# Kernel optimization log

Measured on AMD Instinct MI355X. Metric: run time of the kernel, lower is better.

Reference implementation:

```python
import jax, jax.numpy as jnp
import numpy as np

# eval_para constants (init_kwargs)
RM = 100.0          # r_max
RN = 1000           # r_dsc (radial grid points)
L_MAX = 2
PARA1 = 1.0
RD = RM / RN        # radial step
MR = int(RN * 0.1)  # matching radius index = 100
E_BATCH = 4096

R = jnp.linspace(RM / RN, RM, RN, dtype=jnp.float32).reshape(RN, 1, 1)      # r grid
L = jnp.arange(L_MAX + 1, dtype=jnp.float32).reshape(1, 1, -1)               # l values
FACT = jnp.asarray([np.prod([2 * li + 1 for li in range(lm + 1)])
                    for lm in range(L_MAX + 1)], dtype=jnp.float32)          # (2l+1)!! = [1,3,15]


def disc_solve(sol_init, factor):
    """4th-order Numerov-style recurrence, faithful to the torch loop
    (including the original operator precedence: the 1/(1 - 3/40 rd^2 f[i+4])
    divisor applies only to the sol[i] term)."""
    rd2 = RD * RD
    a = 2.0 + (13.0 / 15.0) * rd2 * factor
    b = -2.0 + (7.0 / 60.0) * rd2 * factor
    c = -1.0 + (3.0 / 40.0) * rd2 * factor
    d = 1.0 - (3.0 / 40.0) * rd2 * factor
    xs = (a[3:RN - 1], b[2:RN - 2], a[1:RN - 3], c[:RN - 4], d[4:])  # each [RN-4, E, L]

    def step(carry, x):
        s0, s1, s2, s3 = carry
        a3, b2, a1, c0, d4 = x
        new = s3 * a3 + s2 * b2 + s1 * a1 + s0 * c0 / d4
        return (s1, s2, s3, new), new

    init = (sol_init[0], sol_init[1], sol_init[2], sol_init[3])
    _, ys = jax.lax.scan(step, init, xs)
    return jnp.concatenate([sol_init[:4], ys], axis=0)


def derivative(f, at):
    # 4th-order backward finite difference
    return (25.0 * f[at] - 48.0 * f[at - 1] + 36.0 * f[at - 2]
            - 16.0 * f[at - 3] + 3.0 * f[at - 4]) / (12.0 * RD)


def integrate_sq(f, n):
    """Faithful port of EvalEig.integrate: n panels of width 4*RD starting at
    index 0 (the original ignores the start offset and leaves f[4i+2] unsquared)."""
    f0 = f[0:4 * n:4]
    f1 = f[1:4 * n + 1:4]
    f2 = f[2:4 * n + 2:4]
    f3 = f[3:4 * n + 3:4]
    f4 = f[4:4 * n + 4:4]
    return ((7.0 * (f0 ** 2 + f4 ** 2) + 32.0 * (f1 ** 2 + f3 ** 2)
             + 12.0 * f2) * (2.0 * RD / 45.0)).sum(0)


def _forward(init_energy):
    E = init_energy.shape[0]
    energy = jnp.broadcast_to(init_energy[:, None], (E, L_MAX + 1))  # [E, L]

    # diffeq_factor with coulomb potential -1/r
    e = energy[None]                                    # [1, E, L]
    factor = L * (L + 1.0) / R ** 2 + PARA1 * (-e - 1.0 / R)  # [RN, E, L]

    # u_zero series initial condition near r=0
    u0_init = jnp.broadcast_to(
        R ** (L + 1.0) + R ** (L + 2.0) / (2.0 * (L + 1.0)) * (-PARA1),
        factor.shape)

    # u_infty initial condition: r * spherical-bessel-like series
    x = R * jnp.sqrt(jnp.abs(e))                        # [RN, E, L]
    base = x ** L / FACT
    h = x * x / 2.0
    series = 1.0 + h / (2.0 * L + 3.0) + h * h / (2.0 * (2.0 * L + 3.0) * (2.0 * L + 5.0))
    ui_init = R * base * series

    # dual propagation: outward and (flipped) inward Numerov scans
    u_zero = disc_solve(u0_init, factor)
    u_infty = jnp.flip(disc_solve(ui_init, jnp.flip(factor, 0)), 0)

    # matching: log-derivative mismatch / norm -> Newton energy step
    lf_in = derivative(u_zero, MR) / u_zero[MR]
    lf_out = derivative(u_infty, MR) / u_infty[MR]
    integ_in = integrate_sq(u_zero, MR // 4 - 1)
    integ_out = integrate_sq(u_infty, (RN - MR) // 4 - 1)
    delta = -(lf_out - lf_in) / (integ_in / u_zero[MR] ** 2 + integ_out / u_infty[MR] ** 2)
    return energy + delta


def setup_inputs() -> dict:
    key = jax.random.key(0)
    init_energy = jax.random.uniform(key, (E_BATCH,), dtype=jnp.float32)
    return {"init_energy": init_energy}


def reference(init_energy) -> jnp.ndarray:
    return _forward(init_energy)
```

## Files before the change

kernel.cpp:

```cpp
#include <hip/hip_runtime.h>
#include <math.h>

#pragma clang fp contract(off)


__device__ __forceinline__ float fmul32(float a, float b) {
  float d; asm("v_mul_f32 %0, %1, %2" : "=v"(d) : "v"(a), "v"(b)); return d;
}
__device__ __forceinline__ float fadd32(float a, float b) {
  float d; asm("v_add_f32 %0, %1, %2" : "=v"(d) : "v"(a), "v"(b)); return d;
}
__device__ __forceinline__ float fsub32(float a, float b) {
  float d; asm("v_sub_f32 %0, %1, %2" : "=v"(d) : "v"(a), "v"(b)); return d;
}
#define FMA32(a, b, c) __builtin_fmaf((a), (b), (c))

#define STEP_TV(TX, TY)                                                        \
  do {                                                                         \
    float f_   = fadd32((TX), fsub32(me, (TY)));                               \
    float ai_  = FMA32(KA32, f_, 2.0f);                                        \
    float bi_  = FMA32(KB32, f_, -2.0f);                                       \
    float di_  = FMA32(nKC32, f_, 1.0f);                     \
    float w_   = fmul32(s0, d_m4) / di_;                   \
    float m2_  = fmul32(s2, b_m2);                                             \
    float t1_  = FMA32(s3, a_m1, m2_);                                         \
    float t2_  = FMA32(s1, a_m3, -w_);           \
    float u_   = fadd32(t1_, t2_);                                             \
    d_m4 = d_m3; d_m3 = d_m2; d_m2 = d_m1; d_m1 = di_;                         \
    a_m3 = a_m2; a_m2 = a_m1; a_m1 = ai_;                                      \
    b_m2 = b_m1; b_m1 = bi_;                                                   \
    s0 = s1; s1 = s2; s2 = s3; s3 = u_;                                        \
  } while (0)

#define STEP(IDX) do { float2 tv_ = tvl[(IDX)]; STEP_TV(tv_.x, tv_.y); } while (0)

__global__ __launch_bounds__(64)
void eval_eig_kernel(const float* __restrict__ ein, float* __restrict__ out, int ntot) {
  constexpr double RD64  = 100.0 / 1000.0;
  constexpr double RD2   = RD64 * RD64;
  constexpr float  KA32  = (float)(13.0 / 15.0 * RD2);
  constexpr float  KB32  = (float)( 7.0 / 60.0 * RD2);
  constexpr float  KC32  = (float)( 3.0 / 40.0 * RD2);
  constexpr float  nKC32 = -KC32;
  constexpr float  DRD32 = (float)(12.0 * RD64);
  constexpr float  ISC32 = (float)(2.0 * RD64 / 45.0);
  constexpr double Q64   = (100.0 - 0.1) / 999.0;

  __shared__ __align__(16) float2 tv[3][1000];
  __shared__ float gbuf[224][64];

  for (int t = threadIdx.x; t < 3000; t += 64) {
    int li = t / 1000, i = t - li * 1000;
    double y = (double)i * Q64 + 0.1;
    float r  = (i == 999) ? 100.0f : (float)y;
    float r2 = fmul32(r, r);
    float num = (float)(li * (li + 1));
    tv[li][i] = make_float2(num / r2, 1.0f / r);
  }
  __syncthreads();

  const int tid = blockIdx.x * 64 + threadIdx.x;
  if (tid >= ntot) return;
  const int b = tid / 3;
  const int l = tid - b * 3;
  const float e  = ein[b];
  const float me = -e;
  const float2* __restrict__ tvl = tv[l];

  float rr[4];
  #pragma unroll
  for (int i = 0; i < 4; ++i) rr[i] = (float)((double)i * Q64 + 0.1);

  auto FVAL = [&](int idx) -> float {
    float2 t_ = tvl[idx];
    return fadd32(t_.x, fsub32(me, t_.y));
  };
  auto PANEL = [&](float f0, float f1, float f2v, float f3, float f4) -> float {
    float s1q = FMA32(f0, f0, fmul32(f4, f4));
    float s3q = FMA32(f1, f1, fmul32(f3, f3));
    float t   = FMA32(7.0f, s1q, fmul32(32.0f, s3q));
    float g   = FMA32(12.0f, f2v, t);
    return fmul32(g, ISC32);
  };
  auto DER5 = [&](float f4, float f3, float f2v, float f1, float f0) -> float {
    float m48 = fmul32(48.0f, f3);
    float d1  = FMA32(25.0f, f4, -m48);
    float d2  = FMA32(36.0f, f2v, d1);
    float d3  = FMA32(-16.0f, f1, d2);
    float d4v = FMA32(3.0f, f0, d3);
    return d4v / DRD32;
  };

  float lf_in, lf_out, integ_in, integ_out, u100v, v899;

  {
    float s0, s1, s2, s3;
    #pragma unroll
    for (int i = 0; i < 4; ++i) {
      double rd = (double)rr[i];
      double r2 = rd * rd;
      float p1, p2;
      if (l == 0)      { p1 = rr[i];            p2 = (float)r2;        }
      else if (l == 1) { p1 = (float)r2;        p2 = (float)(r2 * rd); }
      else             { p1 = (float)(r2 * rd); p2 = (float)(r2 * r2); }
      float q  = p2 / (float)(2 * (l + 1));
      float u0 = fsub32(p1, q);
      if (i == 0) s0 = u0; else if (i == 1) s1 = u0; else if (i == 2) s2 = u0; else s3 = u0;
    }
    float f0 = FVAL(0), f1 = FVAL(1), f2v = FVAL(2), f3 = FVAL(3);
    float a_m1 = FMA32(KA32, f3, 2.0f);
    float a_m2 = FMA32(KA32, f2v, 2.0f);
    float a_m3 = FMA32(KA32, f1, 2.0f);
    float b_m1 = FMA32(KB32, f3, -2.0f);
    float b_m2 = FMA32(KB32, f2v, -2.0f);
    float d_m1 = FMA32(nKC32, f3, 1.0f);
    float d_m2 = FMA32(nKC32, f2v, 1.0f);
    float d_m3 = FMA32(nKC32, f1, 1.0f);
    float d_m4 = FMA32(nKC32, f0, 1.0f);

    float p0 = s0, p1 = s1, p2 = s2, p3 = s3;
    STEP(4);
    float accI = PANEL(p0, p1, p2, p3, s3);
    float pb = s3;
    for (int k = 1; k < 24; ++k) {
      int base = 4 * k;
      STEP(base + 1); float q1 = s3;
      STEP(base + 2); float q2 = s3;
      STEP(base + 3); float q3 = s3;
      STEP(base + 4); float q4 = s3;
      accI = fadd32(accI, PANEL(pb, q1, q2, q3, q4));
      pb = q4;
    }
    float u96 = pb;
    STEP(97);  float u97 = s3;
    STEP(98);  float u98 = s3;
    STEP(99);  float u99 = s3;
    STEP(100); u100v = s3;
    integ_in = accI;
    lf_in = DER5(u100v, u99, u98, u97, u96) / u100v;
  }

  {
    float s0, s1, s2, s3;
    float sq = (float)sqrt((double)fabsf(e));
    #pragma unroll
    for (int i = 0; i < 4; ++i) {
      float x    = fmul32(rr[i], sq);
      float xl   = (l == 0) ? 1.0f : ((l == 1) ? x : fmul32(x, x));
      float fact = (l == 0) ? 1.0f : ((l == 1) ? 3.0f : 15.0f);
      float base = xl / fact;
      float h  = fmul32(x, x) / 2.0f;
      float c1 = (float)(2 * l + 3);
      float c2 = (float)(2 * (2 * l + 3) * (2 * l + 5));
      float t2 = fadd32(1.0f, h / c1);
      float series = fadd32(t2, fmul32(h, h) / c2);
      float ui = fmul32(fmul32(rr[i], base), series);
      if (i == 0) s0 = ui; else if (i == 1) s1 = ui; else if (i == 2) s2 = ui; else s3 = ui;
    }
    float f0 = FVAL(999), f1 = FVAL(998), f2v = FVAL(997), f3 = FVAL(996);
    float a_m1 = FMA32(KA32, f3, 2.0f);
    float a_m2 = FMA32(KA32, f2v, 2.0f);
    float a_m3 = FMA32(KA32, f1, 2.0f);
    float b_m1 = FMA32(KB32, f3, -2.0f);
    float b_m2 = FMA32(KB32, f2v, -2.0f);
    float d_m1 = FMA32(nKC32, f3, 1.0f);
    float d_m2 = FMA32(nKC32, f2v, 1.0f);
    float d_m3 = FMA32(nKC32, f1, 1.0f);
    float d_m4 = FMA32(nKC32, f0, 1.0f);

    #pragma unroll 2
    for (int g = 0; g < 25; ++g) {
      int m0 = 992 - 4 * g;
      const float4* tq = (const float4*)&tvl[m0];
      float4 lo = tq[0], hi = tq[1];
      STEP_TV(hi.z, hi.w);
      STEP_TV(hi.x, hi.y);
      STEP_TV(lo.z, lo.w);
      STEP_TV(lo.x, lo.y);
    }
    float r4v = s3;

    float v900, v901, v902, v903;
    #define BGROUP(P)                                                          \
      const float4* tq = (const float4*)&tvl[4 * (P)];                         \
      float4 lo = tq[0], hi = tq[1];                                           \
      STEP_TV(hi.z, hi.w); float f3v = s3;                                     \
      STEP_TV(hi.x, hi.y); float f2w = s3;                                     \
      STEP_TV(lo.z, lo.w); float f1v = s3;                                     \
      STEP_TV(lo.x, lo.y); float f0v = s3;                                     \
      gbuf[(P)][threadIdx.x] = PANEL(f0v, f1v, f2w, f3v, r4v);                 \
      r4v = f0v;

    #pragma unroll 2
    for (int p = 223; p >= 26; --p) { BGROUP(p); }
    { BGROUP(25); v899 = f0v; }
    { BGROUP(24); v900 = f3v; v901 = f2w; v902 = f1v; v903 = f0v; }
    #pragma unroll 2
    for (int p = 23; p >= 0; --p) { BGROUP(p); }
    #undef BGROUP

    float accO = gbuf[0][threadIdx.x];
    for (int p = 1; p < 224; ++p) accO = fadd32(accO, gbuf[p][threadIdx.x]);
    integ_out = accO;
    lf_out = DER5(v899, v900, v901, v902, v903) / v899;
  }

  float uzsq = fmul32(u100v, u100v);
  float uisq = fmul32(v899, v899);
  float den  = fadd32(integ_in / uzsq, integ_out / uisq);
  float dnum = fsub32(lf_out, lf_in);
  float delta = (-dnum) / den;
  out[tid] = fadd32(e, delta);
}

extern "C" void kernel_launch(void* const* d_in, const int* in_sizes, int n_in,
                              void* d_out, int out_size, void* d_ws, size_t ws_size,
                              hipStream_t stream) {
  const float* ein = (const float*)d_in[0];
  float* out = (float*)d_out;
  int ntot = in_sizes[0] * 3;
  int grid = (ntot + 63) / 64;
  eval_eig_kernel<<<dim3(grid), dim3(64), 0, stream>>>(ein, out, ntot);
}
```

Baseline: 73.41 us.

## Process two independent recurrences per thread to interleave dependency chains

Each thread now runs two (energy, l) Numerov recurrences, A and B, with their steps interleaved. This exposes instruction-level parallelism across two independent serial chains and hides the latency of the divide and FMA chain. It halves the thread count, so the grid shrinks to about 96 blocks of 64, and it doubles the shared panel buffers. That lowers occupancy and CU coverage on a 256-CU part and raises register pressure.

Result: slower. 134.8 us (+83.6%).

```diff
diff --git a/kernel.cpp b/kernel.cpp
--- a/kernel.cpp
+++ b/kernel.cpp
@@ -15,39 +15,104 @@
 }
 #define FMA32(a, b, c) __builtin_fmaf((a), (b), (c))
 
-#define STEP_TV(TX, TY)                                                        \
-  do {                                                                         \
-    float f_   = fadd32((TX), fsub32(me, (TY)));                               \
-    float ai_  = FMA32(KA32, f_, 2.0f);                                        \
-    float bi_  = FMA32(KB32, f_, -2.0f);                                       \
-    float di_  = FMA32(nKC32, f_, 1.0f);                     \
-    float w_   = fmul32(s0, d_m4) / di_;                   \
-    float m2_  = fmul32(s2, b_m2);                                             \
-    float t1_  = FMA32(s3, a_m1, m2_);                                         \
-    float t2_  = FMA32(s1, a_m3, -w_);           \
-    float u_   = fadd32(t1_, t2_);                                             \
-    d_m4 = d_m3; d_m3 = d_m2; d_m2 = d_m1; d_m1 = di_;                         \
-    a_m3 = a_m2; a_m2 = a_m1; a_m1 = ai_;                                      \
-    b_m2 = b_m1; b_m1 = bi_;                                                   \
-    s0 = s1; s1 = s2; s2 = s3; s3 = u_;                                        \
-  } while (0)
-
-#define STEP(IDX) do { float2 tv_ = tvl[(IDX)]; STEP_TV(tv_.x, tv_.y); } while (0)
+constexpr double RD64  = 100.0 / 1000.0;
+constexpr double RD2   = RD64 * RD64;
+constexpr float  KA32  = (float)(13.0 / 15.0 * RD2);
+constexpr float  KB32  = (float)( 7.0 / 60.0 * RD2);
+constexpr float  KC32  = (float)( 3.0 / 40.0 * RD2);
+constexpr float  nKC32 = -KC32;
+constexpr float  DRD32 = (float)(12.0 * RD64);
+constexpr float  ISC32 = (float)(2.0 * RD64 / 45.0);
+constexpr double Q64   = (100.0 - 0.1) / 999.0;
+
+struct CS {
+  float s0, s1, s2, s3;
+  float a1, a2, a3, b1, b2, d1, d2, d3, d4;
+  float me;
+  const float2* tvl;
+};
+
+__device__ __forceinline__ void cstep(CS& c, float tx, float ty) {
+  float f  = fadd32(tx, fsub32(c.me, ty));
+  float ai = FMA32(KA32, f, 2.0f);
+  float bi = FMA32(KB32, f, -2.0f);
+  float di = FMA32(nKC32, f, 1.0f);
+  float w  = fmul32(c.s0, c.d4) / di;
+  float m2 = fmul32(c.s2, c.b2);
+  float t1 = FMA32(c.s3, c.a1, m2);
+  float t2 = FMA32(c.s1, c.a3, -w);
+  float u  = fadd32(t1, t2);
+  c.d4 = c.d3; c.d3 = c.d2; c.d2 = c.d1; c.d1 = di;
+  c.a3 = c.a2; c.a2 = c.a1; c.a1 = ai;
+  c.b2 = c.b1; c.b1 = bi;
+  c.s0 = c.s1; c.s1 = c.s2; c.s2 = c.s3; c.s3 = u;
+}
+__device__ __forceinline__ float fval(const CS& c, int idx) {
+  float2 t = c.tvl[idx];
+  return fadd32(t.x, fsub32(c.me, t.y));
+}
+__device__ __forceinline__ void seed(CS& c, float f0, float f1, float f2, float f3) {
+  c.a1 = FMA32(KA32, f3, 2.0f);  c.a2 = FMA32(KA32, f2, 2.0f);  c.a3 = FMA32(KA32, f1, 2.0f);
+  c.b1 = FMA32(KB32, f3, -2.0f); c.b2 = FMA32(KB32, f2, -2.0f);
+  c.d1 = FMA32(nKC32, f3, 1.0f); c.d2 = FMA32(nKC32, f2, 1.0f);
+  c.d3 = FMA32(nKC32, f1, 1.0f); c.d4 = FMA32(nKC32, f0, 1.0f);
+}
+__device__ __forceinline__ float panel(float f0, float f1, float f2, float f3, float f4) {
+  float s1q = FMA32(f0, f0, fmul32(f4, f4));
+  float s3q = FMA32(f1, f1, fmul32(f3, f3));
+  float t   = FMA32(7.0f, s1q, fmul32(32.0f, s3q));
+  float g   = FMA32(12.0f, f2, t);
+  return fmul32(g, ISC32);
+}
+__device__ __forceinline__ float der5(float f4, float f3, float f2, float f1, float f0) {
+  float m48 = fmul32(48.0f, f3);
+  float d1  = FMA32(25.0f, f4, -m48);
+  float d2  = FMA32(36.0f, f2, d1);
+  float d3  = FMA32(-16.0f, f1, d2);
+  float d4v = FMA32(3.0f, f0, d3);
+  return d4v / DRD32;
+}
+__device__ __forceinline__ void fwd_init(CS& c, int l, const float* rr) {
+  #pragma unroll
+  for (int i = 0; i < 4; ++i) {
+    double rd = (double)rr[i];
+    double r2 = rd * rd;
+    float p1, p2;
+    if (l == 0)      { p1 = rr[i];            p2 = (float)r2;        }
+    else if (l == 1) { p1 = (float)r2;        p2 = (float)(r2 * rd); }
+    else             { p1 = (float)(r2 * rd); p2 = (float)(r2 * r2); }
+    float q  = p2 / (float)(2 * (l + 1));
+    float u0 = fsub32(p1, q);
+    if (i == 0) c.s0 = u0; else if (i == 1) c.s1 = u0;
+    else if (i == 2) c.s2 = u0; else c.s3 = u0;
+  }
+  seed(c, fval(c, 0), fval(c, 1), fval(c, 2), fval(c, 3));
+}
+__device__ __forceinline__ void bwd_init(CS& c, int l, const float* rr, float e) {
+  float sq = (float)sqrt((double)fabsf(e));
+  #pragma unroll
+  for (int i = 0; i < 4; ++i) {
+    float x    = fmul32(rr[i], sq);
+    float xl   = (l == 0) ? 1.0f : ((l == 1) ? x : fmul32(x, x));
+    float fact = (l == 0) ? 1.0f : ((l == 1) ? 3.0f : 15.0f);
+    float base = xl / fact;
+    float h  = fmul32(x, x) / 2.0f;
+    float c1 = (float)(2 * l + 3);
+    float c2 = (float)(2 * (2 * l + 3) * (2 * l + 5));
+    float t2 = fadd32(1.0f, h / c1);
+    float series = fadd32(t2, fmul32(h, h) / c2);
+    float ui = fmul32(fmul32(rr[i], base), series);
+    if (i == 0) c.s0 = ui; else if (i == 1) c.s1 = ui;
+    else if (i == 2) c.s2 = ui; else c.s3 = ui;
+  }
+  seed(c, fval(c, 999), fval(c, 998), fval(c, 997), fval(c, 996));
+}
 
 __global__ __launch_bounds__(64)
 void eval_eig_kernel(const float* __restrict__ ein, float* __restrict__ out, int ntot) {
-  constexpr double RD64  = 100.0 / 1000.0;
-  constexpr double RD2   = RD64 * RD64;
-  constexpr float  KA32  = (float)(13.0 / 15.0 * RD2);
-  constexpr float  KB32  = (float)( 7.0 / 60.0 * RD2);
-  constexpr float  KC32  = (float)( 3.0 / 40.0 * RD2);
-  constexpr float  nKC32 = -KC32;
-  constexpr float  DRD32 = (float)(12.0 * RD64);
-  constexpr float  ISC32 = (float)(2.0 * RD64 / 45.0);
-  constexpr double Q64   = (100.0 - 0.1) / 999.0;
-
   __shared__ __align__(16) float2 tv[3][1000];
-  __shared__ float gbuf[224][64];
+  __shared__ float gbA[224][64];
+  __shared__ float gbB[224][64];
 
   for (int t = threadIdx.x; t < 3000; t += 64) {
     int li = t / 1000, i = t - li * 1000;
@@ -59,158 +124,131 @@
   }
   __syncthreads();
 
-  const int tid = blockIdx.x * 64 + threadIdx.x;
-  if (tid >= ntot) return;
-  const int b = tid / 3;
-  const int l = tid - b * 3;
-  const float e  = ein[b];
-  const float me = -e;
-  const float2* __restrict__ tvl = tv[l];
+  const int gtid = blockIdx.x * 64 + threadIdx.x;
+  const int pA = 2 * gtid;
+  if (pA >= ntot) return;
+  const bool hasB = (pA + 1) < ntot;
+  const int pB = hasB ? (pA + 1) : pA;
+
+  const int bA = pA / 3, lA = pA - bA * 3;
+  const int bB = pB / 3, lB = pB - bB * 3;
+  const float eA = ein[bA], eB = ein[bB];
+
+  CS cA, cB;
+  cA.me = -eA; cA.tvl = tv[lA];
+  cB.me = -eB; cB.tvl = tv[lB];
 
   float rr[4];
   #pragma unroll
   for (int i = 0; i < 4; ++i) rr[i] = (float)((double)i * Q64 + 0.1);
 
-  auto FVAL = [&](int idx) -> float {
-    float2 t_ = tvl[idx];
-    return fadd32(t_.x, fsub32(me, t_.y));
-  };
-  auto PANEL = [&](float f0, float f1, float f2v, float f3, float f4) -> float {
-    float s1q = FMA32(f0, f0, fmul32(f4, f4));
-    float s3q = FMA32(f1, f1, fmul32(f3, f3));
-    float t   = FMA32(7.0f, s1q, fmul32(32.0f, s3q));
-    float g   = FMA32(12.0f, f2v, t);
-    return fmul32(g, ISC32);
-  };
-  auto DER5 = [&](float f4, float f3, float f2v, float f1, float f0) -> float {
-    float m48 = fmul32(48.0f, f3);
-    float d1  = FMA32(25.0f, f4, -m48);
-    float d2  = FMA32(36.0f, f2v, d1);
-    float d3  = FMA32(-16.0f, f1, d2);
-    float d4v = FMA32(3.0f, f0, d3);
-    return d4v / DRD32;
-  };
-
-  float lf_in, lf_out, integ_in, integ_out, u100v, v899;
+  float lf_inA, lf_inB, integ_inA, integ_inB, u100A, u100B;
 
   {
-    float s0, s1, s2, s3;
-    #pragma unroll
-    for (int i = 0; i < 4; ++i) {
-      double rd = (double)rr[i];
-      double r2 = rd * rd;
-      float p1, p2;
-      if (l == 0)      { p1 = rr[i];            p2 = (float)r2;        }
-      else if (l == 1) { p1 = (float)r2;        p2 = (float)(r2 * rd); }
-      else             { p1 = (float)(r2 * rd); p2 = (float)(r2 * r2); }
-      float q  = p2 / (float)(2 * (l + 1));
-      float u0 = fsub32(p1, q);
-      if (i == 0) s0 = u0; else if (i == 1) s1 = u0; else if (i == 2) s2 = u0; else s3 = u0;
-    }
-    float f0 = FVAL(0), f1 = FVAL(1), f2v = FVAL(2), f3 = FVAL(3);
-    float a_m1 = FMA32(KA32, f3, 2.0f);
-    float a_m2 = FMA32(KA32, f2v, 2.0f);
-    float a_m3 = FMA32(KA32, f1, 2.0f);
-    float b_m1 = FMA32(KB32, f3, -2.0f);
-    float b_m2 = FMA32(KB32, f2v, -2.0f);
-    float d_m1 = FMA32(nKC32, f3, 1.0f);
-    float d_m2 = FMA32(nKC32, f2v, 1.0f);
-    float d_m3 = FMA32(nKC32, f1, 1.0f);
-    float d_m4 = FMA32(nKC32, f0, 1.0f);
-
-    float p0 = s0, p1 = s1, p2 = s2, p3 = s3;
-    STEP(4);
-    float accI = PANEL(p0, p1, p2, p3, s3);
-    float pb = s3;
+    fwd_init(cA, lA, rr);
+    fwd_init(cB, lB, rr);
+    float p0A = cA.s0, p1A = cA.s1, p2A = cA.s2, p3A = cA.s3;
+    float p0B = cB.s0, p1B = cB.s1, p2B = cB.s2, p3B = cB.s3;
+    { float2 t = cA.tvl[4]; cstep(cA, t.x, t.y); }
+    { float2 t = cB.tvl[4]; cstep(cB, t.x, t.y); }
+    float accIA = panel(p0A, p1A, p2A, p3A, cA.s3); float pbA = cA.s3;
+    float accIB = panel(p0B, p1B, p2B, p3B, cB.s3); float pbB = cB.s3;
     for (int k = 1; k < 24; ++k) {
       int base = 4 * k;
-      STEP(base + 1); float q1 = s3;
-      STEP(base + 2); float q2 = s3;
-      STEP(base + 3); float q3 = s3;
-      STEP(base + 4); float q4 = s3;
-      accI = fadd32(accI, PANEL(pb, q1, q2, q3, q4));
-      pb = q4;
+      float q1A, q2A, q3A, q4A, q1B, q2B, q3B, q4B;
+      { float2 t = cA.tvl[base + 1]; cstep(cA, t.x, t.y); q1A = cA.s3; }
+      { float2 t = cB.tvl[base + 1]; cstep(cB, t.x, t.y); q1B = cB.s3; }
+      { float2 t = cA.tvl[base + 2]; cstep(cA, t.x, t.y); q2A = cA.s3; }
+      { float2 t = cB.tvl[base + 2]; cstep(cB, t.x, t.y); q2B = cB.s3; }
+      { float2 t = cA.tvl[base + 3]; cstep(cA, t.x, t.y); q3A = cA.s3; }
+      { float2 t = cB.tvl[base + 3]; cstep(cB, t.x, t.y); q3B = cB.s3; }
+      { float2 t = cA.tvl[base + 4]; cstep(cA, t.x, t.y); q4A = cA.s3; }
+      { float2 t = cB.tvl[base + 4]; cstep(cB, t.x, t.y); q4B = cB.s3; }
+      accIA = fadd32(accIA, panel(pbA, q1A, q2A, q3A, q4A)); pbA = q4A;
+      accIB = fadd32(accIB, panel(pbB, q1B, q2B, q3B, q4B)); pbB = q4B;
     }
-    float u96 = pb;
-    STEP(97);  float u97 = s3;
-    STEP(98);  float u98 = s3;
-    STEP(99);  float u99 = s3;
-    STEP(100); u100v = s3;
-    integ_in = accI;
-    lf_in = DER5(u100v, u99, u98, u97, u96) / u100v;
-  }
-
+    float u96A = pbA, u96B = pbB, u97A, u97B, u98A, u98B, u99A, u99B;
+    { float2 t = cA.tvl[97]; cstep(cA, t.x, t.y); u97A = cA.s3; }
+    { float2 t = cB.tvl[97]; cstep(cB, t.x, t.y); u97B = cB.s3; }
+    { float2 t = cA.tvl[98]; cstep(cA, t.x, t.y); u98A = cA.s3; }
+    { float2 t = cB.tvl[98]; cstep(cB, t.x, t.y); u98B = cB.s3; }
+    { float2 t = cA.tvl[99]; cstep(cA, t.x, t.y); u99A = cA.s3; }
+    { float2 t = cB.tvl[99]; cstep(cB, t.x, t.y); u99B = cB.s3; }
+    { float2 t = cA.tvl[100]; cstep(cA, t.x, t.y); u100A = cA.s3; }
+    { float2 t = cB.tvl[100]; cstep(cB, t.x, t.y); u100B = cB.s3; }
+    integ_inA = accIA; integ_inB = accIB;
+    lf_inA = der5(u100A, u99A, u98A, u97A, u96A) / u100A;
+    lf_inB = der5(u100B, u99B, u98B, u97B, u96B) / u100B;
+  }
+
+  float lf_outA, lf_outB, integ_outA, integ_outB, v899A, v899B;
   {
-    float s0, s1, s2, s3;
-    float sq = (float)sqrt((double)fabsf(e));
-    #pragma unroll
-    for (int i = 0; i < 4; ++i) {
-      float x    = fmul32(rr[i], sq);
-      float xl   = (l == 0) ? 1.0f : ((l == 1) ? x : fmul32(x, x));
-      float fact = (l == 0) ? 1.0f : ((l == 1) ? 3.0f : 15.0f);
-      float base = xl / fact;
-      float h  = fmul32(x, x) / 2.0f;
-      float c1 = (float)(2 * l + 3);
-      float c2 = (float)(2 * (2 * l + 3) * (2 * l + 5));
-      float t2 = fadd32(1.0f, h / c1);
-      float series = fadd32(t2, fmul32(h, h) / c2);
-      float ui = fmul32(fmul32(rr[i], base), series);
-      if (i == 0) s0 = ui; else if (i == 1) s1 = ui; else if (i == 2) s2 = ui; else s3 = ui;
-    }
-    float f0 = FVAL(999), f1 = FVAL(998), f2v = FVAL(997), f3 = FVAL(996);
-    float a_m1 = FMA32(KA32, f3, 2.0f);
-    float a_m2 = FMA32(KA32, f2v, 2.0f);
-    float a_m3 = FMA32(KA32, f1, 2.0f);
-    float b_m1 = FMA32(KB32, f3, -2.0f);
-    float b_m2 = FMA32(KB32, f2v, -2.0f);
-    float d_m1 = FMA32(nKC32, f3, 1.0f);
-    float d_m2 = FMA32(nKC32, f2v, 1.0f);
-    float d_m3 = FMA32(nKC32, f1, 1.0f);
-    float d_m4 = FMA32(nKC32, f0, 1.0f);
-
-    #pragma unroll 2
+    bwd_init(cA, lA, rr, eA);
+    bwd_init(cB, lB, rr, eB);
+
     for (int g = 0; g < 25; ++g) {
       int m0 = 992 - 4 * g;
-      const float4* tq = (const float4*)&tvl[m0];
-      float4 lo = tq[0], hi = tq[1];
-      STEP_TV(hi.z, hi.w);
-      STEP_TV(hi.x, hi.y);
-      STEP_TV(lo.z, lo.w);
-      STEP_TV(lo.x, lo.y);
+      float4 la = *(const float4*)&cA.tvl[m0], ha = *(const float4*)&cA.tvl[m0 + 2];
+      float4 lb = *(const float4*)&cB.tvl[m0], hb = *(const float4*)&cB.tvl[m0 + 2];
+      cstep(cA, ha.z, ha.w); cstep(cB, hb.z, hb.w);
+      cstep(cA, ha.x, ha.y); cstep(cB, hb.x, hb.y);
+      cstep(cA, la.z, la.w); cstep(cB, lb.z, lb.w);
+      cstep(cA, la.x, la.y); cstep(cB, lb.x, lb.y);
     }
-    float r4v = s3;
-
-    float v900, v901, v902, v903;
-    #define BGROUP(P)                                                          \
-      const float4* tq = (const float4*)&tvl[4 * (P)];                         \
-      float4 lo = tq[0], hi = tq[1];                                           \
-      STEP_TV(hi.z, hi.w); float f3v = s3;                                     \
-      STEP_TV(hi.x, hi.y); float f2w = s3;                                     \
-      STEP_TV(lo.z, lo.w); float f1v = s3;                                     \
-      STEP_TV(lo.x, lo.y); float f0v = s3;                                     \
-      gbuf[(P)][threadIdx.x] = PANEL(f0v, f1v, f2w, f3v, r4v);                 \
-      r4v = f0v;
-
-    #pragma unroll 2
-    for (int p = 223; p >= 26; --p) { BGROUP(p); }
-    { BGROUP(25); v899 = f0v; }
-    { BGROUP(24); v900 = f3v; v901 = f2w; v902 = f1v; v903 = f0v; }
-    #pragma unroll 2
-    for (int p = 23; p >= 0; --p) { BGROUP(p); }
-    #undef BGROUP
-
-    float accO = gbuf[0][threadIdx.x];
-    for (int p = 1; p < 224; ++p) accO = fadd32(accO, gbuf[p][threadIdx.x]);
-    integ_out = accO;
-    lf_out = DER5(v899, v900, v901, v902, v903) / v899;
-  }
-
-  float uzsq = fmul32(u100v, u100v);
-  float uisq = fmul32(v899, v899);
-  float den  = fadd32(integ_in / uzsq, integ_out / uisq);
-  float dnum = fsub32(lf_out, lf_in);
-  float delta = (-dnum) / den;
-  out[tid] = fadd32(e, delta);
+    float r4A = cA.s3, r4B = cB.s3;
+
+    float v900A, v901A, v902A, v903A, v900B, v901B, v902B, v903B;
+    #define BG2(P)                                                             \
+      float4 la = *(const float4*)&cA.tvl[4 * (P)];                            \
+      float4 ha = *(const float4*)&cA.tvl[4 * (P) + 2];                        \
+      float4 lb = *(const float4*)&cB.tvl[4 * (P)];                            \
+      float4 hb = *(const float4*)&cB.tvl[4 * (P) + 2];                        \
+      cstep(cA, ha.z, ha.w); cstep(cB, hb.z, hb.w);                            \
+      float f3A = cA.s3, f3B = cB.s3;                                          \
+      cstep(cA, ha.x, ha.y); cstep(cB, hb.x, hb.y);                            \
+      float f2A = cA.s3, f2B = cB.s3;                                          \
+      cstep(cA, la.z, la.w); cstep(cB, lb.z, lb.w);                            \
+      float f1A = cA.s3, f1B = cB.s3;                                          \
+      cstep(cA, la.x, la.y); cstep(cB, lb.x, lb.y);                            \
+      float f0A = cA.s3, f0B = cB.s3;                                          \
+      gbA[(P)][threadIdx.x] = panel(f0A, f1A, f2A, f3A, r4A);                  \
+      gbB[(P)][threadIdx.x] = panel(f0B, f1B, f2B, f3B, r4B);                  \
+      r4A = f0A; r4B = f0B;
+
+    for (int p = 223; p >= 26; --p) { BG2(p); }
+    { BG2(25); v899A = f0A; v899B = f0B; }
+    { BG2(24);
+      v900A = f3A; v901A = f2A; v902A = f1A; v903A = f0A;
+      v900B = f3B; v901B = f2B; v902B = f1B; v903B = f0B; }
+    for (int p = 23; p >= 0; --p) { BG2(p); }
+    #undef BG2
+
+    float aA = gbA[0][threadIdx.x], aB = gbB[0][threadIdx.x];
+    for (int p = 1; p < 224; ++p) {
+      aA = fadd32(aA, gbA[p][threadIdx.x]);
+      aB = fadd32(aB, gbB[p][threadIdx.x]);
+    }
+    integ_outA = aA; integ_outB = aB;
+    lf_outA = der5(v899A, v900A, v901A, v902A, v903A) / v899A;
+    lf_outB = der5(v899B, v900B, v901B, v902B, v903B) / v899B;
+  }
+
+  {
+    float uzsq = fmul32(u100A, u100A);
+    float uisq = fmul32(v899A, v899A);
+    float den  = fadd32(integ_inA / uzsq, integ_outA / uisq);
+    float dnum = fsub32(lf_outA, lf_inA);
+    float delta = (-dnum) / den;
+    out[pA] = fadd32(eA, delta);
+  }
+  if (hasB) {
+    float uzsq = fmul32(u100B, u100B);
+    float uisq = fmul32(v899B, v899B);
+    float den  = fadd32(integ_inB / uzsq, integ_outB / uisq);
+    float dnum = fsub32(lf_outB, lf_inB);
+    float delta = (-dnum) / den;
+    out[pB] = fadd32(eB, delta);
+  }
 }
 
 extern "C" void kernel_launch(void* const* d_in, const int* in_sizes, int n_in,
@@ -219,6 +257,7 @@
   const float* ein = (const float*)d_in[0];
   float* out = (float*)d_out;
   int ntot = in_sizes[0] * 3;
-  int grid = (ntot + 63) / 64;
+  int nthread = (ntot + 1) / 2;
+  int grid = (nthread + 63) / 64;
   eval_eig_kernel<<<dim3(grid), dim3(64), 0, stream>>>(ein, out, ntot);
 }
```

## Precompute per-step reciprocal via Newton iteration off the recurrence critical path

Applied to the files above, without the earlier changes.

Replaces the IEEE division in each Numerov step with a reciprocal of the divisor. The reciprocal is computed from rcp plus two Newton refinements, which depend only on the table values and not on the recurrence state, followed by one FMA-based correction of the quotient. This moves the costly divide sequence off the serial dependency chain so coefficients for upcoming steps can be computed ahead. It also drops the inline-asm add/mul wrappers so the compiler can schedule freely, and software-prefetches the next shared-memory table chunk before the current steps run. It risks small rounding differences against exact division and higher register pressure.

New measurement: 62.74 us. 1.17x faster.

```diff
diff --git a/kernel.cpp b/kernel.cpp
--- a/kernel.cpp
+++ b/kernel.cpp
@@ -4,35 +4,10 @@
 #pragma clang fp contract(off)
 
 
-__device__ __forceinline__ float fmul32(float a, float b) {
-  float d; asm("v_mul_f32 %0, %1, %2" : "=v"(d) : "v"(a), "v"(b)); return d;
-}
-__device__ __forceinline__ float fadd32(float a, float b) {
-  float d; asm("v_add_f32 %0, %1, %2" : "=v"(d) : "v"(a), "v"(b)); return d;
-}
-__device__ __forceinline__ float fsub32(float a, float b) {
-  float d; asm("v_sub_f32 %0, %1, %2" : "=v"(d) : "v"(a), "v"(b)); return d;
-}
+__device__ __forceinline__ float fmul32(float a, float b) { return a * b; }
+__device__ __forceinline__ float fadd32(float a, float b) { return a + b; }
+__device__ __forceinline__ float fsub32(float a, float b) { return a - b; }
 #define FMA32(a, b, c) __builtin_fmaf((a), (b), (c))
-
-#define STEP_TV(TX, TY)                                                        \
-  do {                                                                         \
-    float f_   = fadd32((TX), fsub32(me, (TY)));                               \
-    float ai_  = FMA32(KA32, f_, 2.0f);                                        \
-    float bi_  = FMA32(KB32, f_, -2.0f);                                       \
-    float di_  = FMA32(nKC32, f_, 1.0f);                     \
-    float w_   = fmul32(s0, d_m4) / di_;                   \
-    float m2_  = fmul32(s2, b_m2);                                             \
-    float t1_  = FMA32(s3, a_m1, m2_);                                         \
-    float t2_  = FMA32(s1, a_m3, -w_);           \
-    float u_   = fadd32(t1_, t2_);                                             \
-    d_m4 = d_m3; d_m3 = d_m2; d_m2 = d_m1; d_m1 = di_;                         \
-    a_m3 = a_m2; a_m2 = a_m1; a_m1 = ai_;                                      \
-    b_m2 = b_m1; b_m1 = bi_;                                                   \
-    s0 = s1; s1 = s2; s2 = s3; s3 = u_;                                        \
-  } while (0)
-
-#define STEP(IDX) do { float2 tv_ = tvl[(IDX)]; STEP_TV(tv_.x, tv_.y); } while (0)
 
 __global__ __launch_bounds__(64)
 void eval_eig_kernel(const float* __restrict__ ein, float* __restrict__ out, int ntot) {
@@ -67,13 +42,52 @@
   const float me = -e;
   const float2* __restrict__ tvl = tv[l];
 
-  float rr[4];
-  #pragma unroll
-  for (int i = 0; i < 4; ++i) rr[i] = (float)((double)i * Q64 + 0.1);
+  struct Coef { float a, bc, d, y2; };
+  auto MKC = [&](float tx, float ty) -> Coef {
+    Coef c;
+    float f  = fadd32(tx, fsub32(me, ty));
+    c.a  = FMA32(KA32, f, 2.0f);
+    c.bc = FMA32(KB32, f, -2.0f);
+    c.d  = FMA32(nKC32, f, 1.0f);
+    float y0 = __builtin_amdgcn_rcpf(c.d);
+    float e0 = FMA32(-c.d, y0, 1.0f);
+    float y1 = FMA32(y0, e0, y0);
+    float e1 = FMA32(-c.d, y1, 1.0f);
+    c.y2 = FMA32(y1, e1, y1);
+    return c;
+  };
+
+  float s0, s1, s2, s3;
+  float a_m1, a_m2, a_m3, b_m1, b_m2, d_m1, d_m2, d_m3, d_m4;
+  auto CSTEP = [&](const Coef& c) {
+    float n  = fmul32(s0, d_m4);
+    float q0 = fmul32(n, c.y2);
+    float r  = FMA32(-c.d, q0, n);
+    float w  = FMA32(r, c.y2, q0);
+    float m2 = fmul32(s2, b_m2);
+    float t1 = FMA32(s3, a_m1, m2);
+    float t2 = FMA32(s1, a_m3, -w);
+    float u  = fadd32(t1, t2);
+    d_m4 = d_m3; d_m3 = d_m2; d_m2 = d_m1; d_m1 = c.d;
+    a_m3 = a_m2; a_m2 = a_m1; a_m1 = c.a;
+    b_m2 = b_m1; b_m1 = c.bc;
+    s0 = s1; s1 = s2; s2 = s3; s3 = u;
+  };
 
   auto FVAL = [&](int idx) -> float {
     float2 t_ = tvl[idx];
     return fadd32(t_.x, fsub32(me, t_.y));
+  };
+  auto SEED = [&](float f0, float f1, float f2v, float f3) {
+    a_m1 = FMA32(KA32, f3, 2.0f);
+    a_m2 = FMA32(KA32, f2v, 2.0f);
+    a_m3 = FMA32(KA32, f1, 2.0f);
+    b_m1 = FMA32(KB32, f3, -2.0f);
+    b_m2 = FMA32(KB32, f2v, -2.0f);
+    d_m1 = FMA32(nKC32, f3, 1.0f);
+    d_m2 = FMA32(nKC32, f2v, 1.0f);
+    d_m3 = FMA32(nKC32, f1, 1.0f);
+    d_m4 = FMA32(nKC32, f0, 1.0f);
   };
   auto PANEL = [&](float f0, float f1, float f2v, float f3, float f4) -> float {
     float s1q = FMA32(f0, f0, fmul32(f4, f4));
@@ -91,10 +105,13 @@
     return d4v / DRD32;
   };
 
+  float rr[4];
+  #pragma unroll
+  for (int i = 0; i < 4; ++i) rr[i] = (float)((double)i * Q64 + 0.1);
+
   float lf_in, lf_out, integ_in, integ_out, u100v, v899;
 
   {
-    float s0, s1, s2, s3;
     #pragma unroll
     for (int i = 0; i < 4; ++i) {
       double rd = (double)rr[i];
@@ -107,41 +124,39 @@
       float u0 = fsub32(p1, q);
       if (i == 0) s0 = u0; else if (i == 1) s1 = u0; else if (i == 2) s2 = u0; else s3 = u0;
     }
-    float f0 = FVAL(0), f1 = FVAL(1), f2v = FVAL(2), f3 = FVAL(3);
-    float a_m1 = FMA32(KA32, f3, 2.0f);
-    float a_m2 = FMA32(KA32, f2v, 2.0f);
-    float a_m3 = FMA32(KA32, f1, 2.0f);
-    float b_m1 = FMA32(KB32, f3, -2.0f);
-    float b_m2 = FMA32(KB32, f2v, -2.0f);
-    float d_m1 = FMA32(nKC32, f3, 1.0f);
-    float d_m2 = FMA32(nKC32, f2v, 1.0f);
-    float d_m3 = FMA32(nKC32, f1, 1.0f);
-    float d_m4 = FMA32(nKC32, f0, 1.0f);
+    SEED(FVAL(0), FVAL(1), FVAL(2), FVAL(3));
 
     float p0 = s0, p1 = s1, p2 = s2, p3 = s3;
-    STEP(4);
+    { float2 t4 = tvl[4]; Coef c = MKC(t4.x, t4.y); CSTEP(c); }
     float accI = PANEL(p0, p1, p2, p3, s3);
     float pb = s3;
+    #pragma unroll 2
     for (int k = 1; k < 24; ++k) {
       int base = 4 * k;
-      STEP(base + 1); float q1 = s3;
-      STEP(base + 2); float q2 = s3;
-      STEP(base + 3); float q3 = s3;
-      STEP(base + 4); float q4 = s3;
+      float2 t1v = tvl[base + 1], t2v = tvl[base + 2];
+      float2 t3v = tvl[base + 3], t4v = tvl[base + 4];
+      Coef c1 = MKC(t1v.x, t1v.y), c2 = MKC(t2v.x, t2v.y);
+      Coef c3 = MKC(t3v.x, t3v.y), c4 = MKC(t4v.x, t4v.y);
+      CSTEP(c1); float q1 = s3;
+      CSTEP(c2); float q2 = s3;
+      CSTEP(c3); float q3 = s3;
+      CSTEP(c4); float q4 = s3;
       accI = fadd32(accI, PANEL(pb, q1, q2, q3, q4));
       pb = q4;
     }
     float u96 = pb;
-    STEP(97);  float u97 = s3;
-    STEP(98);  float u98 = s3;
-    STEP(99);  float u99 = s3;
-    STEP(100); u100v = s3;
+    float2 t97 = tvl[97], t98 = tvl[98], t99 = tvl[99], t100 = tvl[100];
+    Coef c97 = MKC(t97.x, t97.y), c98 = MKC(t98.x, t98.y);
+    Coef c99 = MKC(t99.x, t99.y), c100 = MKC(t100.x, t100.y);
+    CSTEP(c97);  float u97 = s3;
+    CSTEP(c98);  float u98 = s3;
+    CSTEP(c99);  float u99 = s3;
+    CSTEP(c100); u100v = s3;
     integ_in = accI;
     lf_in = DER5(u100v, u99, u98, u97, u96) / u100v;
   }
 
   {
-    float s0, s1, s2, s3;
     float sq = (float)sqrt((double)fabsf(e));
     #pragma unroll
     for (int i = 0; i < 4; ++i) {
@@ -157,37 +172,37 @@
       float ui = fmul32(fmul32(rr[i], base), series);
       if (i == 0) s0 = ui; else if (i == 1) s1 = ui; else if (i == 2) s2 = ui; else s3 = ui;
     }
-    float f0 = FVAL(999), f1 = FVAL(998), f2v = FVAL(997), f3 = FVAL(996);
-    float a_m1 = FMA32(KA32, f3, 2.0f);
-    float a_m2 = FMA32(KA32, f2v, 2.0f);
-    float a_m3 = FMA32(KA32, f1, 2.0f);
-    float b_m1 = FMA32(KB32, f3, -2.0f);
-    float b_m2 = FMA32(KB32, f2v, -2.0f);
-    float d_m1 = FMA32(nKC32, f3, 1.0f);
-    float d_m2 = FMA32(nKC32, f2v, 1.0f);
-    float d_m3 = FMA32(nKC32, f1, 1.0f);
-    float d_m4 = FMA32(nKC32, f0, 1.0f);
-
+    SEED(FVAL(999), FVAL(998), FVAL(997), FVAL(996));
+
+    float4 lo = *(const float4*)&tvl[992];
+    float4 hi = *(const float4*)&tvl[994];
     #pragma unroll 2
     for (int g = 0; g < 25; ++g) {
-      int m0 = 992 - 4 * g;
-      const float4* tq = (const float4*)&tvl[m0];
-      float4 lo = tq[0], hi = tq[1];
-      STEP_TV(hi.z, hi.w);
-      STEP_TV(hi.x, hi.y);
-      STEP_TV(lo.z, lo.w);
-      STEP_TV(lo.x, lo.y);
+      Coef c3 = MKC(hi.z, hi.w), c2 = MKC(hi.x, hi.y);
+      Coef c1 = MKC(lo.z, lo.w), c0 = MKC(lo.x, lo.y);
+      if (g < 24) {
+        int m0 = 992 - 4 * (g + 1);
+        lo = *(const float4*)&tvl[m0];
+        hi = *(const float4*)&tvl[m0 + 2];
+      }
+      CSTEP(c3); CSTEP(c2); CSTEP(c1); CSTEP(c0);
     }
     float r4v = s3;
 
     float v900, v901, v902, v903;
+    lo = *(const float4*)&tvl[4 * 223];
+    hi = *(const float4*)&tvl[4 * 223 + 2];
     #define BGROUP(P)                                                          \
-      const float4* tq = (const float4*)&tvl[4 * (P)];                         \
-      float4 lo = tq[0], hi = tq[1];                                           \
-      STEP_TV(hi.z, hi.w); float f3v = s3;                                     \
-      STEP_TV(hi.x, hi.y); float f2w = s3;                                     \
-      STEP_TV(lo.z, lo.w); float f1v = s3;                                     \
-      STEP_TV(lo.x, lo.y); float f0v = s3;                                     \
+      Coef c3 = MKC(hi.z, hi.w), c2 = MKC(hi.x, hi.y);                         \
+      Coef c1 = MKC(lo.z, lo.w), c0 = MKC(lo.x, lo.y);                         \
+      if ((P) > 0) {                                                           \
+        lo = *(const float4*)&tvl[4 * (P) - 4];                                \
+        hi = *(const float4*)&tvl[4 * (P) - 2];                                \
+      }                                                                        \
+      CSTEP(c3); float f3v = s3;                                               \
+      CSTEP(c2); float f2w = s3;                                               \
+      CSTEP(c1); float f1v = s3;                                               \
+      CSTEP(c0); float f0v = s3;                                               \
       gbuf[(P)][threadIdx.x] = PANEL(f0v, f1v, f2w, f3v, r4v);                 \
       r4v = f0v;
 
```
